# Performance work log

Hardware: AMD Instinct MI355X
Metric: run time of the kernel (lower is better)

## Reference

```python
import jax, jax.numpy as jnp
import numpy as np

# ----- config (matches init_kwargs) -----
DATA_SIZE = 128
WIDTH = 512
DEPTH = 3          # hidden layers in eqx.nn.MLP
NUM_BLOCKS = 2
BATCH = 512
NSTEPS = 10        # (t1 - t0) / dt0 = 1.0 / 0.1
T1 = 1.0
DT = -0.1          # integrate t1 -> t0

# Tsit5 Butcher tableau (5th-order solution weights; b7 = 0 so stage 7 is skipped)
TS_C = [0.0, 0.161, 0.327, 0.9, 0.9800255409045097, 1.0]
TS_A = [
    [],
    [0.161],
    [-0.008480655492356989, 0.335480655492357],
    [2.8971530571054935, -6.359448489975075, 4.3622954328695815],
    [5.325864828439257, -11.748883564062828, 7.4955393428898365, -0.09249506636175525],
    [5.86145544294642, -12.92096931784711, 8.159367898576159, -0.071584973281401, -0.028269050394068383],
]
TS_B = [0.09646076681806523, 0.01, 0.4798896504144996, 1.379008574103742, -3.290069515436081, 2.324710524099774]


def setup_inputs() -> dict:
    key = jax.random.key(0)
    ks = jax.random.split(key, 10)
    d, w, nb = DATA_SIZE, WIDTH, NUM_BLOCKS
    in0 = d + 1  # autonomous=False: t is concatenated to y

    def init(k, shape, fan_in):
        return jax.random.normal(k, shape, dtype=jnp.float32) / np.sqrt(fan_in).astype(np.float32)

    return {
        "y": jax.random.normal(ks[0], (BATCH, d), dtype=jnp.float32),
        "Ws0": init(ks[1], (nb, in0, w), in0), "bs0": init(ks[2], (nb, w), w),
        "Ws1": init(ks[3], (nb, w, w), w),     "bs1": init(ks[4], (nb, w), w),
        "Ws2": init(ks[5], (nb, w, w), w),     "bs2": init(ks[6], (nb, w), w),
        "Ws3": init(ks[7], (nb, w, d), w),     "bs3": init(ks[8], (nb, d), d),
    }


def _mlp(inp, layers):
    # inp: [in_size] vector (per-sample), relu hidden activations, linear output
    h = inp
    for W, b in layers[:-1]:
        h = jax.nn.relu(h @ W + b)
    W, b = layers[-1]
    return h @ W + b


def _field_and_trace(t, y, layers):
    # y: [B, d]. Exact log-det trace via vmapped vjp over identity (exact_logp_wrapper).
    eye = jnp.eye(DATA_SIZE, dtype=y.dtype)

    def single(yy):
        fn = lambda z: _mlp(jnp.concatenate([jnp.full((1,), t, yy.dtype), z]), layers)
        f, vjp_fn = jax.vjp(fn, yy)
        (dfdy,) = jax.vmap(vjp_fn)(eye)  # [d, d] Jacobian
        return f, jnp.trace(dfdy)

    return jax.vmap(single)(y)


def _solve_block(y, lp, layers):
    # Fixed-step Tsit5 on augmented state (y, logp), t1 -> t0, 10 steps.
    def step(carry, n):
        y, lp = carry
        t = jnp.float32(T1) + jnp.float32(DT) * n.astype(jnp.float32)
        ky, klp = [], []
        for i in range(6):
            ti = t + jnp.float32(TS_C[i] * DT)
            yi = y
            for j in range(i):
                yi = yi + jnp.float32(DT * TS_A[i][j]) * ky[j]
            fy, flp = _field_and_trace(ti, yi, layers)
            ky.append(fy)
            klp.append(flp)
        for i in range(6):
            y = y + jnp.float32(DT * TS_B[i]) * ky[i]
            lp = lp + jnp.float32(DT * TS_B[i]) * klp[i]
        return (y, lp), None

    (y, lp), _ = jax.lax.scan(step, (y, lp), jnp.arange(NSTEPS))
    return y, lp


def reference(y, Ws0, bs0, Ws1, bs1, Ws2, bs2, Ws3, bs3):
    lp = jnp.zeros((y.shape[0],), dtype=y.dtype)  # delta log-likelihood
    for b in range(NUM_BLOCKS):
        layers = [(Ws0[b], bs0[b]), (Ws1[b], bs1[b]), (Ws2[b], bs2[b]), (Ws3[b], bs3[b])]
        y, lp = _solve_block(y, lp, layers)
    # normal_log_likelihood (faithful to source: log(2*pi) NOT scaled by d)
    log2pi = np.float32(np.log(2.0 * np.pi))
    return lp + (-0.5) * (log2pi + jnp.sum(y * y, axis=-1))
```

## Files before the change

### kernel.cpp

```cpp
#include <hip/hip_runtime.h>


using short8 = __attribute__((ext_vector_type(8))) short;
using u16x8  = __attribute__((ext_vector_type(8))) unsigned short;
using f32x4v = __attribute__((ext_vector_type(4))) float;
using i32x4  = __attribute__((ext_vector_type(4))) int;
using u32x4  = __attribute__((ext_vector_type(4))) unsigned;
using i32x16 = __attribute__((ext_vector_type(16))) int;

__device__ __forceinline__ unsigned short f2bf(float f) {
  union { float f; unsigned u; } v; v.f = f;
  unsigned r = v.u + 0x7fffu + ((v.u >> 16) & 1u);
  return (unsigned short)(r >> 16);
}
__device__ __forceinline__ float bf2f(unsigned short h) {
  union { unsigned u; float f; } v; v.u = ((unsigned)h) << 16; return v.f;
}
__device__ __forceinline__ signed char q8(float v, float inv) {
  float r = rintf(v * inv);
  r = fminf(fmaxf(r, -127.f), 127.f);
  return (signed char)(int)r;
}

typedef const __attribute__((address_space(1))) void gas_t;
typedef __attribute__((address_space(3))) void las_t;
__device__ __forceinline__ void gl_lds16(const void* g, void* l) {
  __builtin_amdgcn_global_load_lds((gas_t*)g, (las_t*)l, 16, 0, 0);
}

struct Coef5 { float v[5]; };
struct Coef6 { float v[6]; };

#define INV_S0 254.0f
#define INV_S1 508.0f
#define SCALE_J 7.7500155e-06f
#define SCALE_G 3.8750077e-06f

__global__ __launch_bounds__(256) void init_state(const float* __restrict__ y_in,
                                                  float* __restrict__ y,
                                                  float* __restrict__ lp) {
  int i = blockIdx.x * 256 + threadIdx.x;
  if (i < 512 * 128) y[i] = y_in[i];
  if (i < 512) lp[i] = 0.f;
}

__global__ __launch_bounds__(256) void cast_weights(
    const float* __restrict__ W0, const float* __restrict__ W1,
    const float* __restrict__ W2, const float* __restrict__ W3,
    signed char* __restrict__ w0q,
    unsigned short* __restrict__ w0tH, unsigned short* __restrict__ w0tL,
    unsigned short* __restrict__ w1tH, unsigned short* __restrict__ w1tL,
    signed char* __restrict__ w1q,
    unsigned short* __restrict__ w2tH, unsigned short* __restrict__ w2tL,
    unsigned short* __restrict__ w3tH, unsigned short* __restrict__ w3tL,
    signed char* __restrict__ w3q, signed char* __restrict__ w2q) {
  int i = blockIdx.x * 256 + threadIdx.x;
  if (i < 65536) {
    int j = i >> 9, a = i & 511;
    w0q[i] = q8(W0[(1 + j) * 512 + a], INV_S0);
    return;
  }
  i -= 65536;
  if (i >= 2 * 65536 + 2 * 262144) {
    int q = i - (2 * 65536 + 2 * 262144);
    if (q < 262144) w2q[q] = q8(W2[q], INV_S1);
    return;
  }
  float v;
  unsigned short* dh;
  unsigned short* dl;
  signed char* qd = nullptr;
  int di;
  if (i < 65536) {
    int n = i >> 7, k = i & 127;
    v = W0[(1 + k) * 512 + n]; dh = w0tH; dl = w0tL; di = i;
  } else if (i < 65536 + 262144) {
    int q = i - 65536; int n = q >> 9, k = q & 511;
    v = W1[k * 512 + n]; dh = w1tH; dl = w1tL; di = q; qd = w1q;
  } else if (i < 65536 + 2 * 262144) {
    int q = i - 65536 - 262144; int c = q >> 9, b = q & 511;
    v = W2[b * 512 + c]; dh = w2tH; dl = w2tL; di = q;
  } else {
    int q = i - 65536 - 2 * 262144; int j = q >> 9, c = q & 511;
    v = W3[c * 128 + j]; dh = w3tH; dl = w3tL; di = q; qd = w3q;
  }
  unsigned short hi = f2bf(v);
  dh[di] = hi;
  dl[di] = f2bf(v - bf2f(hi));
  if (qd) qd[di] = q8(v, INV_S1);
}

__global__ __launch_bounds__(256, 2) void fwd_l0(
    const float* __restrict__ yb, const float* __restrict__ kyb, Coef5 ca, int nc,
    const unsigned short* __restrict__ WtH, const unsigned short* __restrict__ WtL,
    const float* __restrict__ bias, const float* __restrict__ wrow0, float tval,
    unsigned short* __restrict__ Hhi, unsigned short* __restrict__ Hlo) {
  __shared__ unsigned short AsH[4096], AsL[4096], BsH[4096], BsL[4096];
  const int t = threadIdx.x, l = t & 63;
  const int wv = t >> 6, wm = wv >> 1, wn = wv & 1;
  const int lr = l & 15, lg = l >> 4, lr7 = lr & 7;
  const int m0 = blockIdx.y * 32, n0 = blockIdx.x * 32;

#pragma unroll
  for (int r = 0; r < 2; ++r) {
    int g = r * 256 + t;
    int row = g >> 4;
    int gc = (g & 15) ^ (row & 7);
    size_t bo = (size_t)(n0 + row) * 128 + gc * 8;
    int db = (r * 256 + (t & 192)) * 16;
    gl_lds16(WtH + bo, (char*)BsH + db);
    gl_lds16(WtL + bo, (char*)BsL + db);
  }
  {
    int row = t >> 3, seg = t & 7;
    int gidx = (m0 + row) * 128 + seg * 16;
    float x[16];
#pragma unroll
    for (int q = 0; q < 4; ++q) *(float4*)&x[q * 4] = *(const float4*)&yb[gidx + q * 4];
    for (int j2 = 0; j2 < nc; ++j2) {
      float c = ca.v[j2];
#pragma unroll
      for (int q = 0; q < 4; ++q) {
        float4 u = *(const float4*)&kyb[j2 * 65536 + gidx + q * 4];
        x[q * 4 + 0] = fmaf(c, u.x, x[q * 4 + 0]);
        x[q * 4 + 1] = fmaf(c, u.y, x[q * 4 + 1]);
        x[q * 4 + 2] = fmaf(c, u.z, x[q * 4 + 2]);
        x[q * 4 + 3] = fmaf(c, u.w, x[q * 4 + 3]);
      }
    }
    u16x8 h8[2], l8[2];
#pragma unroll
    for (int e = 0; e < 16; ++e) {
      unsigned short hh = f2bf(x[e]);
      h8[e >> 3][e & 7] = hh;
      l8[e >> 3][e & 7] = f2bf(x[e] - bf2f(hh));
    }
#pragma unroll
    for (int h = 0; h < 2; ++h) {
      int gx = (seg * 2 + h) ^ (row & 7);
      *(u16x8*)((char*)AsH + row * 256 + gx * 16) = h8[h];
      *(u16x8*)((char*)AsL + row * 256 + gx * 16) = l8[h];
    }
  }
  __syncthreads();

  f32x4v acc = {0.f, 0.f, 0.f, 0.f};
#pragma unroll
  for (int ks = 0; ks < 4; ++ks) {
    int sl = ((ks * 4 + lg) ^ lr7) << 4;
    int ab = (wm * 16 + lr) * 256 + sl;
    int bb = (wn * 16 + lr) * 256 + sl;
    short8 ah = *(const short8*)((const char*)AsH + ab);
    short8 al = *(const short8*)((const char*)AsL + ab);
    short8 bh = *(const short8*)((const char*)BsH + bb);
    short8 bl = *(const short8*)((const char*)BsL + bb);
    acc = __builtin_amdgcn_mfma_f32_16x16x32_bf16(ah, bh, acc, 0, 0, 0);
    acc = __builtin_amdgcn_mfma_f32_16x16x32_bf16(ah, bl, acc, 0, 0, 0);
    acc = __builtin_amdgcn_mfma_f32_16x16x32_bf16(al, bh, acc, 0, 0, 0);
  }

  int n = n0 + wn * 16 + lr;
  float be = fmaf(tval, wrow0[n], bias[n]);
#pragma unroll
  for (int r = 0; r < 4; ++r) {
    int m = m0 + wm * 16 + lg * 4 + r;
    float v = fmaxf(acc[r] + be, 0.f);
    unsigned short h = f2bf(v);
    Hhi[m * 512 + n] = h;
    Hlo[m * 512 + n] = f2bf(v - bf2f(h));
  }
}

template <bool RELU>
__global__ __launch_bounds__(256, 2) void fwd_mfma(
    const unsigned short* __restrict__ Ahi, const unsigned short* __restrict__ Alo,
    const unsigned short* __restrict__ WtH, const unsigned short* __restrict__ WtL,
    const float* __restrict__ bias,
    float* __restrict__ Cf, unsigned short* __restrict__ Hhi,
    unsigned short* __restrict__ Hlo, int N, int K) {
  __shared__ unsigned short AsH[2][4096], AsL[2][4096], BsH[2][4096], BsL[2][4096];
  const int t = threadIdx.x, l = t & 63, w = t >> 6;
  const int wm = w >> 1, wn = w & 1, lr = l & 15, lg = l >> 4;
  const int m0 = blockIdx.y * 32, n0 = blockIdx.x * 32;
  const int lr7 = lr & 7;

  auto stage = [&](int cur, int k0) {
#pragma unroll
    for (int r = 0; r < 2; ++r) {
      int g = r * 256 + t;
      int row = g >> 4, gc = g & 15;
      size_t co = (size_t)k0 + ((gc ^ (row & 7)) << 3);
      size_t ao = (size_t)(m0 + row) * K + co;
      size_t bo = (size_t)(n0 + row) * K + co;
      int db = (r * 256 + (t & 192)) * 16;
      gl_lds16(Ahi + ao, (char*)AsH[cur] + db);
      gl_lds16(Alo + ao, (char*)AsL[cur] + db);
      gl_lds16(WtH + bo, (char*)BsH[cur] + db);
      gl_lds16(WtL + bo, (char*)BsL[cur] + db);
    }
  };

  f32x4v acc = {0.f, 0.f, 0.f, 0.f};
  stage(0, 0);
  __syncthreads();
  int cur = 0;
  for (int k0 = 0; k0 < K; k0 += 128) {
    if (k0 + 128 < K) stage(cur ^ 1, k0 + 128);
#pragma unroll
    for (int ks = 0; ks < 4; ++ks) {
      int sl = ((ks * 4 + lg) ^ lr7) << 4;
      int ab = (wm * 16 + lr) * 256 + sl;
      int bb = (wn * 16 + lr) * 256 + sl;
      short8 ah = *(const short8*)((const char*)AsH[cur] + ab);
      short8 al = *(const short8*)((const char*)AsL[cur] + ab);
      short8 bh = *(const short8*)((const char*)BsH[cur] + bb);
      short8 bl = *(const short8*)((const char*)BsL[cur] + bb);
      acc = __builtin_amdgcn_mfma_f32_16x16x32_bf16(ah, bh, acc, 0, 0, 0);
      acc = __builtin_amdgcn_mfma_f32_16x16x32_bf16(ah, bl, acc, 0, 0, 0);
      acc = __builtin_amdgcn_mfma_f32_16x16x32_bf16(al, bh, acc, 0, 0, 0);
    }
    __syncthreads();
    cur ^= 1;
  }

  int n = n0 + wn * 16 + lr;
  float be = bias[n];
#pragma unroll
  for (int r = 0; r < 4; ++r) {
    int m = m0 + wm * 16 + lg * 4 + r;
    float v = acc[r] + be;
    if (RELU) {
      v = fmaxf(v, 0.f);
      unsigned short h = f2bf(v);
      Hhi[m * N + n] = h;
      Hlo[m * N + n] = f2bf(v - bf2f(h));
    } else {
      Cf[m * N + n] = v;
    }
  }
}

__global__ __launch_bounds__(256, 2) void jac_fused(
    const signed char* __restrict__ w1q, const signed char* __restrict__ w0q,
    const signed char* __restrict__ w2q, const signed char* __restrict__ w3q,
    const unsigned short* __restrict__ d0m, const unsigned short* __restrict__ d1m,
    const unsigned short* __restrict__ d2m, float* __restrict__ klp) {
  __shared__ signed char As[2][8192];
  __shared__ signed char Bs[2][8192];
  __shared__ unsigned char Ms8[3 * 2 * 512];
  __shared__ float red[8];
  const int cb = blockIdx.x, s0 = blockIdx.y * 2;
  const int t = threadIdx.x, l = t & 63, w = t >> 6;
  const int wm = w >> 1, wn = w & 1;
  const int lr31 = l & 31, hi = l >> 5;

  if (w < 3) {
    const unsigned short* src = (w == 0) ? d0m : (w == 1) ? d1m : d2m;
    gl_lds16(src + (size_t)s0 * 512 + l * 8, (void*)&As[0][w * 2048]);
    gl_lds16(src + (size_t)(s0 + 1) * 512 + l * 8, (void*)&As[0][w * 2048 + 1024]);
  }
  __syncthreads();
  {
    const unsigned* Mraw = (const unsigned*)&As[0][0];
    unsigned* Mout = (unsigned*)&Ms8[0];
#pragma unroll
    for (int q = 0; q < 3; ++q) {
      int i = q * 256 + t;
      unsigned lo = Mraw[2 * i], hi2 = Mraw[2 * i + 1];
      unsigned m = 0;
      if (lo & 0xFFFFu) m |= 0x000000FFu;
      if (lo >> 16)     m |= 0x0000FF00u;
      if (hi2 & 0xFFFFu) m |= 0x00FF0000u;
      if (hi2 >> 16)     m |= 0xFF000000u;
      Mout[i] = m;
    }
  }
  __syncthreads();

  auto stage = [&](int buf, const signed char* Aq, const signed char* Bq, int k0) {
#pragma unroll
    for (int i = 0; i < 4; ++i) {
      int u = i * 4 + w;
      int uu = (u < 8) ? u : (u - 8);
      int g = uu * 64 + l;
      int row = g & 127;
      int kh = (g >> 7) & 1;
      int ks = g >> 8;
      int kb = k0 + ks * 32 + kh * 16;
      if (u < 8) {
        gl_lds16(Aq + (size_t)(cb * 128 + row) * 512 + kb,
                 (void*)&As[buf][uu * 1024]);
      } else {
        gl_lds16(Bq + (size_t)row * 512 + kb, (void*)&Bs[buf][uu * 1024]);
      }
    }
  };

  i32x16 a0[2][2], a1[2][2];
  auto phase = [&](const signed char* Aq, const signed char* Bq, int mbase) {
#pragma unroll
    for (int mt = 0; mt < 2; ++mt)
#pragma unroll
      for (int nt = 0; nt < 2; ++nt) {
        a0[mt][nt] = (i32x16)(0);
        a1[mt][nt] = (i32x16)(0);
      }
    stage(0, Aq, Bq, 0);
    __syncthreads();
    int cur = 0;
    for (int k0 = 0; k0 < 512; k0 += 64) {
      if (k0 + 64 < 512) stage(cur ^ 1, Aq, Bq, k0 + 64);
#pragma unroll
      for (int ks = 0; ks < 2; ++ks) {
        i32x4 af[2];
#pragma unroll
        for (int mt = 0; mt < 2; ++mt)
          af[mt] = *(const i32x4*)&As[cur][(ks * 256 + hi * 128 +
                                            wm * 64 + mt * 32 + lr31) * 16];
        u32x4 mk0 = *(const u32x4*)&Ms8[mbase + k0 + ks * 32 + hi * 16];
        u32x4 mk1 = *(const u32x4*)&Ms8[mbase + 512 + k0 + ks * 32 + hi * 16];
#pragma unroll
        for (int nt = 0; nt < 2; ++nt) {
          u32x4 bv = *(const u32x4*)&Bs[cur][(ks * 256 + hi * 128 +
                                              wn * 64 + nt * 32 + lr31) * 16];
          i32x4 b0 = (i32x4)(bv & mk0);
          i32x4 b1 = (i32x4)(bv & mk1);
#pragma unroll
          for (int mt = 0; mt < 2; ++mt) {
            a0[mt][nt] = __builtin_amdgcn_mfma_i32_32x32x32_i8(af[mt], b0,
                                                               a0[mt][nt], 0, 0, 0);
            a1[mt][nt] = __builtin_amdgcn_mfma_i32_32x32x32_i8(af[mt], b1,
                                                               a1[mt][nt], 0, 0, 0);
          }
        }
      }
      __syncthreads();
      cur ^= 1;
    }
  };

  phase(w2q, w3q, 2 * 1024);
  unsigned pg0[2][2][8], pg1[2][2][8];
#pragma unroll
  for (int mt = 0; mt < 2; ++mt)
#pragma unroll
    for (int nt = 0; nt < 2; ++nt)
#pragma unroll
      for (int p = 0; p < 8; ++p) {
        float ga = (float)a0[mt][nt][2 * p] * SCALE_G;
        float gb = (float)a0[mt][nt][2 * p + 1] * SCALE_G;
        float gc = (float)a1[mt][nt][2 * p] * SCALE_G;
        float gd = (float)a1[mt][nt][2 * p + 1] * SCALE_G;
        asm("v_cvt_pk_bf16_f32 %0, %1, %2" : "=v"(pg0[mt][nt][p]) : "v"(ga), "v"(gb));
        asm("v_cvt_pk_bf16_f32 %0, %1, %2" : "=v"(pg1[mt][nt][p]) : "v"(gc), "v"(gd));
      }

  phase(w1q, w0q, 0);

  float p0 = 0.f, p1 = 0.f;
  const unsigned char* D1b = &Ms8[1 * 1024];
#pragma unroll
  for (int mt = 0; mt < 2; ++mt) {
#pragma unroll
    for (int q = 0; q < 4; ++q) {
      int blg = cb * 128 + wm * 64 + mt * 32 + q * 8 + 4 * hi;
      uchar4 m40 = *(const uchar4*)&D1b[blg];
      uchar4 m41 = *(const uchar4*)&D1b[512 + blg];
      unsigned char mm0[4] = {m40.x, m40.y, m40.z, m40.w};
      unsigned char mm1[4] = {m41.x, m41.y, m41.z, m41.w};
#pragma unroll
      for (int e = 0; e < 4; ++e) {
        const int r = q * 4 + e;
#pragma unroll
        for (int nt = 0; nt < 2; ++nt) {
          unsigned pw0 = pg0[mt][nt][r >> 1];
          unsigned pw1 = pg1[mt][nt][r >> 1];
          unsigned short g0 = (r & 1) ? (unsigned short)(pw0 >> 16)
                                      : (unsigned short)(pw0 & 0xFFFFu);
          unsigned short g1 = (r & 1) ? (unsigned short)(pw1 >> 16)
                                      : (unsigned short)(pw1 & 0xFFFFu);
          if (mm0[e]) p0 = fmaf((float)a0[mt][nt][r], bf2f(g0), p0);
          if (mm1[e]) p1 = fmaf((float)a1[mt][nt][r], bf2f(g1), p1);
        }
      }
    }
  }
  p0 *= SCALE_J;
  p1 *= SCALE_J;
#pragma unroll
  for (int off = 1; off < 64; off <<= 1) {
    p0 += __shfl_xor(p0, off);
    p1 += __shfl_xor(p1, off);
  }
  if (l == 0) { red[w * 2] = p0; red[w * 2 + 1] = p1; }
  __syncthreads();
  if (t < 2) {
    klp[cb * 512 + s0 + t] = red[t] + red[2 + t] + red[4 + t] + red[6 + t];
  }
}

__global__ __launch_bounds__(256) void step_update(float* __restrict__ y,
                                                   float* __restrict__ lp,
                                                   const float* __restrict__ ky,
                                                   const float* __restrict__ klp_part,
                                                   Coef6 db) {
  int i = blockIdx.x * 256 + threadIdx.x;
  if (i < 65536) {
    float a = y[i];
#pragma unroll
    for (int j = 0; j < 6; ++j) a += db.v[j] * ky[j * 65536 + i];
    y[i] = a;
  }
  if (i < 512) {
    float l = lp[i];
#pragma unroll
    for (int j = 0; j < 6; ++j) {
      const float* kp = klp_part + j * 2048;
      float tr = kp[i] + kp[512 + i] + kp[1024 + i] + kp[1536 + i];
      l += db.v[j] * tr;
    }
    lp[i] = l;
  }
}

__global__ __launch_bounds__(64) void finalize(const float* __restrict__ y,
                                               const float* __restrict__ lp,
                                               float* __restrict__ out) {
  int s = blockIdx.x, l = threadIdx.x;
  float v0 = y[s * 128 + l], v1 = y[s * 128 + 64 + l];
  float sum = v0 * v0 + v1 * v1;
#pragma unroll
  for (int off = 32; off; off >>= 1) sum += __shfl_down(sum, off);
  if (l == 0) out[s] = lp[s] + (-0.5f) * (1.8378770664093453f + sum);
}

extern "C" void kernel_launch(void* const* d_in, const int* in_sizes, int n_in,
                              void* d_out, int out_size, void* d_ws, size_t ws_size,
                              hipStream_t stream) {
  const float* y_in = (const float*)d_in[0];
  const float* Ws0 = (const float*)d_in[1];
  const float* bs0 = (const float*)d_in[2];
  const float* Ws1 = (const float*)d_in[3];
  const float* bs1 = (const float*)d_in[4];
  const float* Ws2 = (const float*)d_in[5];
  const float* bs2 = (const float*)d_in[6];
  const float* Ws3 = (const float*)d_in[7];
  const float* bs3 = (const float*)d_in[8];
  float* out = (float*)d_out;

  char* ws = (char*)d_ws;
  size_t off = 0;
  auto alloc = [&](size_t bytes) {
    void* p = ws + off;
    off = (off + bytes + 255) & ~(size_t)255;
    return p;
  };
  float* y  = (float*)alloc(65536 * 4);
  float* lp = (float*)alloc(512 * 4);
  unsigned short* h0hi = (unsigned short*)alloc(262144 * 2);
  unsigned short* h0lo = (unsigned short*)alloc(262144 * 2);
  unsigned short* h1hi = (unsigned short*)alloc(262144 * 2);
  unsigned short* h1lo = (unsigned short*)alloc(262144 * 2);
  unsigned short* h2hi = (unsigned short*)alloc(262144 * 2);
  unsigned short* h2lo = (unsigned short*)alloc(262144 * 2);
  float* ky  = (float*)alloc(6 * 65536 * 4);
  float* klp = (float*)alloc(6 * 2048 * 4);
  unsigned short* w0tH = (unsigned short*)alloc(65536 * 2);
  unsigned short* w0tL = (unsigned short*)alloc(65536 * 2);
  unsigned short* w1tH = (unsigned short*)alloc(262144 * 2);
  unsigned short* w1tL = (unsigned short*)alloc(262144 * 2);
  unsigned short* w2tH = (unsigned short*)alloc(262144 * 2);
  unsigned short* w2tL = (unsigned short*)alloc(262144 * 2);
  unsigned short* w3tH = (unsigned short*)alloc(65536 * 2);
  unsigned short* w3tL = (unsigned short*)alloc(65536 * 2);
  signed char* w0q = (signed char*)alloc(65536);
  signed char* w1q = (signed char*)alloc(262144);
  signed char* w2q = (signed char*)alloc(262144);
  signed char* w3q = (signed char*)alloc(65536);
  (void)ws_size; (void)in_sizes; (void)n_in; (void)out_size;

  static const double DT = -0.1;
  static const double TC[6] = {0.0, 0.161, 0.327, 0.9, 0.9800255409045097, 1.0};
  static const double TA[6][5] = {
      {0, 0, 0, 0, 0},
      {0.161, 0, 0, 0, 0},
      {-0.008480655492356989, 0.335480655492357, 0, 0, 0},
      {2.8971530571054935, -6.359448489975075, 4.3622954328695815, 0, 0},
      {5.325864828439257, -11.748883564062828, 7.4955393428898365, -0.09249506636175525, 0},
      {5.86145544294642, -12.92096931784711, 8.159367898576159, -0.071584973281401,
       -0.028269050394068383}};
  static const double TB[6] = {0.09646076681806523, 0.01, 0.4798896504144996,
                               1.379008574103742, -3.290069515436081, 2.324710524099774};

  init_state<<<dim3(256), dim3(256), 0, stream>>>(y_in, y, lp);

  for (int blk = 0; blk < 2; ++blk) {
    const float* W0 = Ws0 + blk * 129 * 512;
    const float* b0 = bs0 + blk * 512;
    const float* W1 = Ws1 + blk * 262144;
    const float* b1 = bs1 + blk * 512;
    const float* W2 = Ws2 + blk * 262144;
    const float* b2 = bs2 + blk * 512;
    const float* W3 = Ws3 + blk * 65536;
    const float* b3 = bs3 + blk * 128;

    cast_weights<<<dim3(3840), dim3(256), 0, stream>>>(
        W0, W1, W2, W3, w0q, w0tH, w0tL, w1tH, w1tL, w1q,
        w2tH, w2tL, w3tH, w3tL, w3q, w2q);

    for (int n = 0; n < 10; ++n) {
      float t = 1.0f + (-0.1f) * (float)n;
      for (int i = 0; i < 6; ++i) {
        float ti = t + (float)(TC[i] * DT);
        Coef5 ca;
        for (int j = 0; j < 5; ++j) ca.v[j] = (j < i) ? (float)(DT * TA[i][j]) : 0.f;

        fwd_l0<<<dim3(16, 16), 256, 0, stream>>>(
            y, ky, ca, i, w0tH, w0tL, b0, W0, ti, h0hi, h0lo);
        fwd_mfma<true><<<dim3(16, 16), 256, 0, stream>>>(
            h0hi, h0lo, w1tH, w1tL, b1, nullptr, h1hi, h1lo, 512, 512);
        fwd_mfma<true><<<dim3(16, 16), 256, 0, stream>>>(
            h1hi, h1lo, w2tH, w2tL, b2, nullptr, h2hi, h2lo, 512, 512);
        fwd_mfma<false><<<dim3(4, 16), 256, 0, stream>>>(
            h2hi, h2lo, w3tH, w3tL, b3, ky + i * 65536, nullptr, nullptr, 128, 512);
        jac_fused<<<dim3(4, 256), 256, 0, stream>>>(
            w1q, w0q, w2q, w3q, h0hi, h1hi, h2hi, klp + i * 2048);
      }
      Coef6 db;
      for (int i2 = 0; i2 < 6; ++i2) db.v[i2] = (float)(DT * TB[i2]);
      step_update<<<dim3(256), dim3(256), 0, stream>>>(y, lp, ky, klp, db);
    }
  }
  finalize<<<dim3(512), dim3(64), 0, stream>>>(y, lp, out);
}
```

Baseline: 7.882 ms.

## Fuse next-stage layer-0 forward into Jacobian kernel and double the Jacobian K tile

The separate layer-0 forward kernel is folded into the Jacobian-trace launch as extra blocks. Those blocks compute the next Runge-Kutta stage's first hidden layer into a double-buffered h0, while the remaining blocks compute the current stage's trace. On the last stage of a step, the final Tsit5 weights are used so the next step's input is formed without waiting for step_update. The int8 Jacobian GEMM also stages 128-wide K tiles instead of 64, which raises shared memory to about 68 KB per block and may limit occupancy.

Measured after the change: 7.388 ms. 1.07x faster.

```diff
diff --git a/kernel.cpp b/kernel.cpp
--- a/kernel.cpp
+++ b/kernel.cpp
@@ -28,7 +28,6 @@
   __builtin_amdgcn_global_load_lds((gas_t*)g, (las_t*)l, 16, 0, 0);
 }
 
-struct Coef5 { float v[5]; };
 struct Coef6 { float v[6]; };
 
 #define INV_S0 254.0f
@@ -90,87 +89,6 @@
   if (qd) qd[di] = q8(v, INV_S1);
 }
 
-__global__ __launch_bounds__(256, 2) void fwd_l0(
-    const float* __restrict__ yb, const float* __restrict__ kyb, Coef5 ca, int nc,
-    const unsigned short* __restrict__ WtH, const unsigned short* __restrict__ WtL,
-    const float* __restrict__ bias, const float* __restrict__ wrow0, float tval,
-    unsigned short* __restrict__ Hhi, unsigned short* __restrict__ Hlo) {
-  __shared__ unsigned short AsH[4096], AsL[4096], BsH[4096], BsL[4096];
-  const int t = threadIdx.x, l = t & 63;
-  const int wv = t >> 6, wm = wv >> 1, wn = wv & 1;
-  const int lr = l & 15, lg = l >> 4, lr7 = lr & 7;
-  const int m0 = blockIdx.y * 32, n0 = blockIdx.x * 32;
-
-#pragma unroll
-  for (int r = 0; r < 2; ++r) {
-    int g = r * 256 + t;
-    int row = g >> 4;
-    int gc = (g & 15) ^ (row & 7);
-    size_t bo = (size_t)(n0 + row) * 128 + gc * 8;
-    int db = (r * 256 + (t & 192)) * 16;
-    gl_lds16(WtH + bo, (char*)BsH + db);
-    gl_lds16(WtL + bo, (char*)BsL + db);
-  }
-  {
-    int row = t >> 3, seg = t & 7;
-    int gidx = (m0 + row) * 128 + seg * 16;
-    float x[16];
-#pragma unroll
-    for (int q = 0; q < 4; ++q) *(float4*)&x[q * 4] = *(const float4*)&yb[gidx + q * 4];
-    for (int j2 = 0; j2 < nc; ++j2) {
-      float c = ca.v[j2];
-#pragma unroll
-      for (int q = 0; q < 4; ++q) {
-        float4 u = *(const float4*)&kyb[j2 * 65536 + gidx + q * 4];
-        x[q * 4 + 0] = fmaf(c, u.x, x[q * 4 + 0]);
-        x[q * 4 + 1] = fmaf(c, u.y, x[q * 4 + 1]);
-        x[q * 4 + 2] = fmaf(c, u.z, x[q * 4 + 2]);
-        x[q * 4 + 3] = fmaf(c, u.w, x[q * 4 + 3]);
-      }
-    }
-    u16x8 h8[2], l8[2];
-#pragma unroll
-    for (int e = 0; e < 16; ++e) {
-      unsigned short hh = f2bf(x[e]);
-      h8[e >> 3][e & 7] = hh;
-      l8[e >> 3][e & 7] = f2bf(x[e] - bf2f(hh));
-    }
-#pragma unroll
-    for (int h = 0; h < 2; ++h) {
-      int gx = (seg * 2 + h) ^ (row & 7);
-      *(u16x8*)((char*)AsH + row * 256 + gx * 16) = h8[h];
-      *(u16x8*)((char*)AsL + row * 256 + gx * 16) = l8[h];
-    }
-  }
-  __syncthreads();
-
-  f32x4v acc = {0.f, 0.f, 0.f, 0.f};
-#pragma unroll
-  for (int ks = 0; ks < 4; ++ks) {
-    int sl = ((ks * 4 + lg) ^ lr7) << 4;
-    int ab = (wm * 16 + lr) * 256 + sl;
-    int bb = (wn * 16 + lr) * 256 + sl;
-    short8 ah = *(const short8*)((const char*)AsH + ab);
-    short8 al = *(const short8*)((const char*)AsL + ab);
-    short8 bh = *(const short8*)((const char*)BsH + bb);
-    short8 bl = *(const short8*)((const char*)BsL + bb);
-    acc = __builtin_amdgcn_mfma_f32_16x16x32_bf16(ah, bh, acc, 0, 0, 0);
-    acc = __builtin_amdgcn_mfma_f32_16x16x32_bf16(ah, bl, acc, 0, 0, 0);
-    acc = __builtin_amdgcn_mfma_f32_16x16x32_bf16(al, bh, acc, 0, 0, 0);
-  }
-
-  int n = n0 + wn * 16 + lr;
-  float be = fmaf(tval, wrow0[n], bias[n]);
-#pragma unroll
-  for (int r = 0; r < 4; ++r) {
-    int m = m0 + wm * 16 + lg * 4 + r;
-    float v = fmaxf(acc[r] + be, 0.f);
-    unsigned short h = f2bf(v);
-    Hhi[m * 512 + n] = h;
-    Hlo[m * 512 + n] = f2bf(v - bf2f(h));
-  }
-}
-
 template <bool RELU>
 __global__ __launch_bounds__(256, 2) void fwd_mfma(
     const unsigned short* __restrict__ Ahi, const unsigned short* __restrict__ Alo,
@@ -240,29 +158,118 @@
   }
 }
 
-__global__ __launch_bounds__(256, 2) void jac_fused(
+__global__ __launch_bounds__(256, 2) void jac_l0(
+    int l0n,
     const signed char* __restrict__ w1q, const signed char* __restrict__ w0q,
     const signed char* __restrict__ w2q, const signed char* __restrict__ w3q,
     const unsigned short* __restrict__ d0m, const unsigned short* __restrict__ d1m,
-    const unsigned short* __restrict__ d2m, float* __restrict__ klp) {
-  __shared__ signed char As[2][8192];
-  __shared__ signed char Bs[2][8192];
-  __shared__ unsigned char Ms8[3 * 2 * 512];
-  __shared__ float red[8];
-  const int cb = blockIdx.x, s0 = blockIdx.y * 2;
+    const unsigned short* __restrict__ d2m, float* __restrict__ klp,
+    const float* __restrict__ yb, const float* __restrict__ kyb, Coef6 ca, int nc,
+    const unsigned short* __restrict__ WtH, const unsigned short* __restrict__ WtL,
+    const float* __restrict__ bias, const float* __restrict__ wrow0, float tval,
+    unsigned short* __restrict__ Hhi, unsigned short* __restrict__ Hlo) {
+  __shared__ __align__(16) char smraw[68672];
   const int t = threadIdx.x, l = t & 63, w = t >> 6;
+
+  if ((int)blockIdx.x < l0n) {
+    unsigned short* AsH = (unsigned short*)(smraw);
+    unsigned short* AsL = (unsigned short*)(smraw + 8192);
+    unsigned short* BsH = (unsigned short*)(smraw + 16384);
+    unsigned short* BsL = (unsigned short*)(smraw + 24576);
+    const int lb = blockIdx.x;
+    const int wm = w >> 1, wn = w & 1, lr = l & 15, lg = l >> 4, lr7 = lr & 7;
+    const int m0 = (lb >> 4) * 32, n0 = (lb & 15) * 32;
+
+#pragma unroll
+    for (int r = 0; r < 2; ++r) {
+      int g = r * 256 + t;
+      int row = g >> 4;
+      int gc = (g & 15) ^ (row & 7);
+      size_t bo = (size_t)(n0 + row) * 128 + gc * 8;
+      int db = (r * 256 + (t & 192)) * 16;
+      gl_lds16(WtH + bo, (char*)BsH + db);
+      gl_lds16(WtL + bo, (char*)BsL + db);
+    }
+    {
+      int row = t >> 3, seg = t & 7;
+      int gidx = (m0 + row) * 128 + seg * 16;
+      float x[16];
+#pragma unroll
+      for (int q = 0; q < 4; ++q)
+        *(float4*)&x[q * 4] = *(const float4*)&yb[gidx + q * 4];
+      for (int j2 = 0; j2 < nc; ++j2) {
+        float c = ca.v[j2];
+#pragma unroll
+        for (int q = 0; q < 4; ++q) {
+          float4 u = *(const float4*)&kyb[j2 * 65536 + gidx + q * 4];
+          x[q * 4 + 0] = fmaf(c, u.x, x[q * 4 + 0]);
+          x[q * 4 + 1] = fmaf(c, u.y, x[q * 4 + 1]);
+          x[q * 4 + 2] = fmaf(c, u.z, x[q * 4 + 2]);
+          x[q * 4 + 3] = fmaf(c, u.w, x[q * 4 + 3]);
+        }
+      }
+      u16x8 h8[2], l8[2];
+#pragma unroll
+      for (int e = 0; e < 16; ++e) {
+        unsigned short hh = f2bf(x[e]);
+        h8[e >> 3][e & 7] = hh;
+        l8[e >> 3][e & 7] = f2bf(x[e] - bf2f(hh));
+      }
+#pragma unroll
+      for (int h = 0; h < 2; ++h) {
+        int gx = (seg * 2 + h) ^ (row & 7);
+        *(u16x8*)((char*)AsH + row * 256 + gx * 16) = h8[h];
+        *(u16x8*)((char*)AsL + row * 256 + gx * 16) = l8[h];
+      }
+    }
+    __syncthreads();
+
+    f32x4v acc = {0.f, 0.f, 0.f, 0.f};
+#pragma unroll
+    for (int ks = 0; ks < 4; ++ks) {
+      int sl = ((ks * 4 + lg) ^ lr7) << 4;
+      int ab = (wm * 16 + lr) * 256 + sl;
+      int bb = (wn * 16 + lr) * 256 + sl;
+      short8 ah = *(const short8*)((const char*)AsH + ab);
+      short8 al = *(const short8*)((const char*)AsL + ab);
+      short8 bh = *(const short8*)((const char*)BsH + bb);
+      short8 bl = *(const short8*)((const char*)BsL + bb);
+      acc = __builtin_amdgcn_mfma_f32_16x16x32_bf16(ah, bh, acc, 0, 0, 0);
+      acc = __builtin_amdgcn_mfma_f32_16x16x32_bf16(ah, bl, acc, 0, 0, 0);
+      acc = __builtin_amdgcn_mfma_f32_16x16x32_bf16(al, bh, acc, 0, 0, 0);
+    }
+
+    int n = n0 + wn * 16 + lr;
+    float be = fmaf(tval, wrow0[n], bias[n]);
+#pragma unroll
+    for (int r = 0; r < 4; ++r) {
+      int m = m0 + wm * 16 + lg * 4 + r;
+      float v = fmaxf(acc[r] + be, 0.f);
+      unsigned short h = f2bf(v);
+      Hhi[m * 512 + n] = h;
+      Hlo[m * 512 + n] = f2bf(v - bf2f(h));
+    }
+    return;
+  }
+
+  signed char* As = (signed char*)smraw;
+  signed char* Bs = (signed char*)(smraw + 32768);
+  unsigned char* Ms8 = (unsigned char*)(smraw + 65536);
+  float* red = (float*)(smraw + 68608);
+  const int jx = blockIdx.x - l0n;
+  const int cb = jx & 3, s0 = (jx >> 2) * 2;
   const int wm = w >> 1, wn = w & 1;
   const int lr31 = l & 31, hi = l >> 5;
 
   if (w < 3) {
     const unsigned short* src = (w == 0) ? d0m : (w == 1) ? d1m : d2m;
-    gl_lds16(src + (size_t)s0 * 512 + l * 8, (void*)&As[0][w * 2048]);
-    gl_lds16(src + (size_t)(s0 + 1) * 512 + l * 8, (void*)&As[0][w * 2048 + 1024]);
+    gl_lds16(src + (size_t)s0 * 512 + l * 8, As + w * 2048);
+    gl_lds16(src + (size_t)(s0 + 1) * 512 + l * 8, As + w * 2048 + 1024);
   }
   __syncthreads();
   {
-    const unsigned* Mraw = (const unsigned*)&As[0][0];
-    unsigned* Mout = (unsigned*)&Ms8[0];
+    const unsigned* Mraw = (const unsigned*)As;
+    unsigned* Mout = (unsigned*)Ms8;
 #pragma unroll
     for (int q = 0; q < 3; ++q) {
       int i = q * 256 + t;
@@ -279,20 +286,18 @@
 
   auto stage = [&](int buf, const signed char* Aq, const signed char* Bq, int k0) {
 #pragma unroll
-    for (int i = 0; i < 4; ++i) {
+    for (int i = 0; i < 8; ++i) {
       int u = i * 4 + w;
-      int uu = (u < 8) ? u : (u - 8);
+      int uu = (u < 16) ? u : (u - 16);
       int g = uu * 64 + l;
       int row = g & 127;
       int kh = (g >> 7) & 1;
       int ks = g >> 8;
       int kb = k0 + ks * 32 + kh * 16;
-      if (u < 8) {
-        gl_lds16(Aq + (size_t)(cb * 128 + row) * 512 + kb,
-                 (void*)&As[buf][uu * 1024]);
-      } else {
-        gl_lds16(Bq + (size_t)row * 512 + kb, (void*)&Bs[buf][uu * 1024]);
-      }
+      if (u < 16)
+        gl_lds16(Aq + (size_t)(cb * 128 + row) * 512 + kb, As + buf * 16384 + uu * 1024);
+      else
+        gl_lds16(Bq + (size_t)row * 512 + kb, Bs + buf * 16384 + uu * 1024);
     }
   };
 
@@ -308,21 +313,21 @@
     stage(0, Aq, Bq, 0);
     __syncthreads();
     int cur = 0;
-    for (int k0 = 0; k0 < 512; k0 += 64) {
-      if (k0 + 64 < 512) stage(cur ^ 1, Aq, Bq, k0 + 64);
-#pragma unroll
-      for (int ks = 0; ks < 2; ++ks) {
+    for (int k0 = 0; k0 < 512; k0 += 128) {
+      if (k0 + 128 < 512) stage(cur ^ 1, Aq, Bq, k0 + 128);
+#pragma unroll
+      for (int ks = 0; ks < 4; ++ks) {
         i32x4 af[2];
 #pragma unroll
         for (int mt = 0; mt < 2; ++mt)
-          af[mt] = *(const i32x4*)&As[cur][(ks * 256 + hi * 128 +
-                                            wm * 64 + mt * 32 + lr31) * 16];
+          af[mt] = *(const i32x4*)(As + cur * 16384 +
+                                   (ks * 256 + hi * 128 + wm * 64 + mt * 32 + lr31) * 16);
         u32x4 mk0 = *(const u32x4*)&Ms8[mbase + k0 + ks * 32 + hi * 16];
         u32x4 mk1 = *(const u32x4*)&Ms8[mbase + 512 + k0 + ks * 32 + hi * 16];
 #pragma unroll
         for (int nt = 0; nt < 2; ++nt) {
-          u32x4 bv = *(const u32x4*)&Bs[cur][(ks * 256 + hi * 128 +
-                                              wn * 64 + nt * 32 + lr31) * 16];
+          u32x4 bv = *(const u32x4*)(Bs + cur * 16384 +
+                                     (ks * 256 + hi * 128 + wn * 64 + nt * 32 + lr31) * 16);
           i32x4 b0 = (i32x4)(bv & mk0);
           i32x4 b1 = (i32x4)(bv & mk1);
 #pragma unroll
@@ -457,8 +462,10 @@
   };
   float* y  = (float*)alloc(65536 * 4);
   float* lp = (float*)alloc(512 * 4);
-  unsigned short* h0hi = (unsigned short*)alloc(262144 * 2);
-  unsigned short* h0lo = (unsigned short*)alloc(262144 * 2);
+  unsigned short* h0hi[2] = {(unsigned short*)alloc(262144 * 2),
+                             (unsigned short*)alloc(262144 * 2)};
+  unsigned short* h0lo[2] = {(unsigned short*)alloc(262144 * 2),
+                             (unsigned short*)alloc(262144 * 2)};
   unsigned short* h1hi = (unsigned short*)alloc(262144 * 2);
   unsigned short* h1lo = (unsigned short*)alloc(262144 * 2);
   unsigned short* h2hi = (unsigned short*)alloc(262144 * 2);
@@ -492,6 +499,9 @@
   static const double TB[6] = {0.09646076681806523, 0.01, 0.4798896504144996,
                                1.379008574103742, -3.290069515436081, 2.324710524099774};
 
+  Coef6 db;
+  for (int i2 = 0; i2 < 6; ++i2) db.v[i2] = (float)(DT * TB[i2]);
+
   init_state<<<dim3(256), dim3(256), 0, stream>>>(y_in, y, lp);
 
   for (int blk = 0; blk < 2; ++blk) {
@@ -509,25 +519,41 @@
         w2tH, w2tL, w3tH, w3tL, w3q, w2q);
 
     for (int n = 0; n < 10; ++n) {
-      float t = 1.0f + (-0.1f) * (float)n;
+      float tn = 1.0f + (-0.1f) * (float)n;
       for (int i = 0; i < 6; ++i) {
-        float ti = t + (float)(TC[i] * DT);
-        Coef5 ca;
-        for (int j = 0; j < 5; ++j) ca.v[j] = (j < i) ? (float)(DT * TA[i][j]) : 0.f;
-
-        fwd_l0<<<dim3(16, 16), 256, 0, stream>>>(
-            y, ky, ca, i, w0tH, w0tL, b0, W0, ti, h0hi, h0lo);
+        const int p = i & 1;
+        if (n == 0 && i == 0) {
+          Coef6 c0 = {{0, 0, 0, 0, 0, 0}};
+          jac_l0<<<dim3(256), 256, 0, stream>>>(
+              256, w1q, w0q, w2q, w3q, h0hi[0], h1hi, h2hi, klp,
+              y, ky, c0, 0, w0tH, w0tL, b0, W0, tn, h0hi[0], h0lo[0]);
+        }
         fwd_mfma<true><<<dim3(16, 16), 256, 0, stream>>>(
-            h0hi, h0lo, w1tH, w1tL, b1, nullptr, h1hi, h1lo, 512, 512);
+            h0hi[p], h0lo[p], w1tH, w1tL, b1, nullptr, h1hi, h1lo, 512, 512);
         fwd_mfma<true><<<dim3(16, 16), 256, 0, stream>>>(
             h1hi, h1lo, w2tH, w2tL, b2, nullptr, h2hi, h2lo, 512, 512);
         fwd_mfma<false><<<dim3(4, 16), 256, 0, stream>>>(
             h2hi, h2lo, w3tH, w3tL, b3, ky + i * 65536, nullptr, nullptr, 128, 512);
-        jac_fused<<<dim3(4, 256), 256, 0, stream>>>(
-            w1q, w0q, w2q, w3q, h0hi, h1hi, h2hi, klp + i * 2048);
-      }
-      Coef6 db;
-      for (int i2 = 0; i2 < 6; ++i2) db.v[i2] = (float)(DT * TB[i2]);
+
+        if (i < 5) {
+          Coef6 cn = {{0, 0, 0, 0, 0, 0}};
+          for (int j = 0; j <= i; ++j) cn.v[j] = (float)(DT * TA[i + 1][j]);
+          float tin = tn + (float)(TC[i + 1] * DT);
+          jac_l0<<<dim3(1280), 256, 0, stream>>>(
+              256, w1q, w0q, w2q, w3q, h0hi[p], h1hi, h2hi, klp + i * 2048,
+              y, ky, cn, i + 1, w0tH, w0tL, b0, W0, tin, h0hi[p ^ 1], h0lo[p ^ 1]);
+        } else if (n < 9) {
+          float tin = tn - 0.1f;
+          jac_l0<<<dim3(1280), 256, 0, stream>>>(
+              256, w1q, w0q, w2q, w3q, h0hi[p], h1hi, h2hi, klp + 5 * 2048,
+              y, ky, db, 6, w0tH, w0tL, b0, W0, tin, h0hi[p ^ 1], h0lo[p ^ 1]);
+        } else {
+          Coef6 c0 = {{0, 0, 0, 0, 0, 0}};
+          jac_l0<<<dim3(1024), 256, 0, stream>>>(
+              0, w1q, w0q, w2q, w3q, h0hi[p], h1hi, h2hi, klp + 5 * 2048,
+              y, ky, c0, 0, w0tH, w0tL, b0, W0, tn, h0hi[p ^ 1], h0lo[p ^ 1]);
+        }
+      }
       step_update<<<dim3(256), dim3(256), 0, stream>>>(y, lp, ky, klp, db);
     }
   }
```
